# Optimization experiments

Measured on AMD Instinct MI355X. Metric: run time of the kernel, lower is better.

## Reference

```python
import jax, jax.numpy as jnp
import numpy as np

MARGIN = 0.3


def setup_inputs() -> dict:
    key = jax.random.key(0)
    k1, k2 = jax.random.split(key)
    embeddings = jax.random.normal(k1, (128, 512, 1024), dtype=jnp.float32)
    labels = jax.random.randint(k2, (128, 512), 0, 2, dtype=jnp.int64)
    return {"embeddings": embeddings, "labels": labels}


def reference(embeddings, labels):
    # L2-normalize each item embedding (F.normalize, dim=-1)
    emb = embeddings / jnp.linalg.norm(embeddings, axis=-1, keepdims=True)  # [B,N,D]
    dt = emb.dtype

    # Per-sample cosine similarity matrices.
    sim = jnp.einsum('bnd,bmd->bnm', emb, emb)  # [B,N,N]
    diag = jnp.einsum('bnd,bnd->bn', emb, emb)  # [B,N], ~1 after normalization

    pos = labels == 1
    neg = labels == 0
    posf = pos.astype(dt)  # [B,N]
    negf = neg.astype(dt)
    n_pos = pos.sum(-1)  # [B]
    n_neg = neg.sum(-1)

    # Mean similarity of each positive anchor to the OTHER positives
    # (exclude self via diag; original concatenates around p_idx).
    pos_sum = jnp.einsum('bnm,bm->bn', sim, posf) - diag  # [B,N]
    denom_pos = jnp.maximum(n_pos[:, None].astype(dt) - 1, 1)
    pos_sim = jnp.where(n_pos[:, None] > 1, pos_sum / denom_pos, jnp.asarray(1.0, dt))  # [B,N]

    # relu(neg_sim - pos_sim + margin), mean over negatives per anchor.
    tri = jax.nn.relu(sim - pos_sim[:, :, None] + MARGIN)  # [B,N,N]
    denom_neg = jnp.maximum(n_neg[:, None].astype(dt), 1)
    neg_mean = jnp.einsum('bnm,bm->bn', tri, negf) / denom_neg  # [B,N]

    # Only samples with both positives and negatives contribute; one term per positive anchor.
    valid = (n_pos > 0) & (n_neg > 0)  # [B]
    anchor_w = posf * valid[:, None].astype(dt)  # [B,N]
    total = (neg_mean * anchor_w).sum()
    count = (n_pos * valid).sum()
    return total / jnp.maximum(count, 1).astype(dt)
```

## Files before the change

kernel.cpp:

```cpp
#include <hip/hip_runtime.h>
#include <hip/hip_bf16.h>

#define BB 128
#define NN 512
#define DD 1024
#define MARGIN 0.3f

typedef __attribute__((ext_vector_type(8))) short bf16x8;
typedef __attribute__((ext_vector_type(4))) float f32x4;
typedef __attribute__((ext_vector_type(8))) unsigned short ushort8;
typedef long i64f8;

__device__ __forceinline__ unsigned short f2bf(float f) {
    unsigned int u = __float_as_uint(f);
    u += 0x7FFFu + ((u >> 16) & 1u);
    return (unsigned short)(u >> 16);
}
__device__ __forceinline__ int read_label(const unsigned int* lab, int is64, int idx) {
    return (int)(is64 ? lab[2 * idx] : lab[idx]);
}
__device__ __forceinline__ void gload_lds16(const void* g, void* l) {
    __builtin_amdgcn_global_load_lds(
        (const __attribute__((address_space(1))) unsigned int*)g,
        (__attribute__((address_space(3))) unsigned int*)l, 16, 0, 0);
}


__global__ __launch_bounds__(512) void k_compact2(const unsigned int* __restrict__ lab,
                                                  int* __restrict__ slotOf,
                                                  int* __restrict__ counts) {
    int b = blockIdx.x, t = threadIdx.x;
    int lnk = t & 63, wv = t >> 6;

    unsigned int odd = (t < 256) ? lab[2 * (b * 256 + t) + 1] : 0u;
    #pragma unroll
    for (int off = 32; off; off >>= 1) odd |= __shfl_xor(odd, off);
    __shared__ unsigned int ow[8];
    if (lnk == 0) ow[wv] = odd;
    __syncthreads();
    unsigned int tot = ow[0] | ow[1] | ow[2] | ow[3] | ow[4] | ow[5] | ow[6] | ow[7];
    int is64 = (tot == 0) ? 1 : 0;

    int lv = read_label(lab, is64, b * NN + t);
    unsigned long long bp = __ballot(lv == 1);
    int prefP = __popcll(bp & ((1ull << lnk) - 1ull));
    __shared__ int wcP[8];
    if (lnk == 0) wcP[wv] = __popcll(bp);
    __syncthreads();
    int baseP = 0, totP = 0;
    #pragma unroll
    for (int w = 0; w < 8; ++w) {
        int c = wcP[w];
        if (w < wv) baseP += c;
        totP += c;
    }
    int baseN = wv * 64 - baseP;
    int prefN = lnk - prefP;
    int slot = (lv == 1) ? (baseP + prefP) : (totP + baseN + prefN);
    slotOf[b * NN + t] = slot;
    if (t == 0) { counts[2 * b] = totP; counts[2 * b + 1] = NN - totP; }
}

#define TM 128
#define TN 128
__global__ __launch_bounds__(128) void k_tiles(const int* __restrict__ counts,
                                               int* __restrict__ tileList,
                                               int* __restrict__ nTiles) {
    int b = threadIdx.x;
    int P = counts[2 * b], Q = counts[2 * b + 1];
    int nm = (P > 0) ? (P + TM - 1) / TM : 0;
    int nn = (Q > 0) ? (Q + TN - 1) / TN : 0;
    int cnt = nm * nn;
    __shared__ int pre[128];
    pre[b] = cnt;
    __syncthreads();
    for (int d = 1; d < 128; d <<= 1) {
        int v = (b >= d) ? pre[b - d] : 0;
        __syncthreads();
        pre[b] += v;
        __syncthreads();
    }
    int off = pre[b] - cnt;
    for (int mt = 0; mt < nm; ++mt)
        for (int nt = 0; nt < nn; ++nt)
            tileList[off++] = (b << 8) | (mt << 4) | nt;
    if (b == 127) nTiles[0] = pre[127];
}

__global__ __launch_bounds__(256) void k_normcvt(const float* __restrict__ x,
                                                 const int* __restrict__ slotOf,
                                                 unsigned char* __restrict__ y8) {
    int wid = blockIdx.x * 4 + (threadIdx.x >> 6);
    int ln = threadIdx.x & 63;
    const f32x4* src = (const f32x4*)(x + (size_t)wid * DD);
    f32x4 v[4];
    float ss = 0.f;
    #pragma unroll
    for (int j = 0; j < 4; ++j) {
        v[j] = __builtin_nontemporal_load(&src[ln + 64 * j]);
        ss += v[j].x * v[j].x + v[j].y * v[j].y + v[j].z * v[j].z + v[j].w * v[j].w;
    }
    #pragma unroll
    for (int off = 32; off; off >>= 1) ss += __shfl_xor(ss, off);
    float r = rsqrtf(ss);
    int b = wid >> 9;
    int slot = slotOf[wid];
    unsigned char* dst = y8 + ((size_t)(b * NN) + slot) * DD;
    #pragma unroll
    for (int j = 0; j < 4; ++j) {
        int w = 0;
        w = __builtin_amdgcn_cvt_pk_fp8_f32(v[j].x * r, v[j].y * r, w, false);
        w = __builtin_amdgcn_cvt_pk_fp8_f32(v[j].z * r, v[j].w * r, w, true);
        *(unsigned int*)&dst[4 * (ln + 64 * j)] = (unsigned int)w;
    }
}

__global__ __launch_bounds__(256) void k_spos2(const unsigned char* __restrict__ y8,
                                               const int* __restrict__ counts,
                                               float* __restrict__ sposPart) {
    int blk = blockIdx.x;
    int b = blk >> 3, sub = blk & 7;
    int t = threadIdx.x, wv = t >> 6, ln = t & 63;
    int P = counts[2 * b];
    int lo = (sub * P) >> 3, hi = ((sub + 1) * P) >> 3;
    const unsigned char* yb = y8 + (size_t)b * NN * DD;
    float acc[16];
    #pragma unroll
    for (int e = 0; e < 16; ++e) acc[e] = 0.f;
    for (int s = lo + wv; s < hi; s += 4) {
        uint4 w = *(const uint4*)(yb + (size_t)s * DD + 16 * ln);
        unsigned int wa[4] = {w.x, w.y, w.z, w.w};
        #pragma unroll
        for (int i = 0; i < 4; ++i) {
            acc[4 * i + 0] += __builtin_amdgcn_cvt_f32_fp8(wa[i], 0);
            acc[4 * i + 1] += __builtin_amdgcn_cvt_f32_fp8(wa[i], 1);
            acc[4 * i + 2] += __builtin_amdgcn_cvt_f32_fp8(wa[i], 2);
            acc[4 * i + 3] += __builtin_amdgcn_cvt_f32_fp8(wa[i], 3);
        }
    }
    __shared__ float part[4][1024];
    #pragma unroll
    for (int i = 0; i < 4; ++i)
        *(float4*)&part[wv][16 * ln + 4 * i] =
            make_float4(acc[4 * i], acc[4 * i + 1], acc[4 * i + 2], acc[4 * i + 3]);
    __syncthreads();
    float* outp = sposPart + (size_t)blk * DD;
    #pragma unroll
    for (int g = 0; g < 4; ++g) {
        int c = t + 256 * g;
        outp[c] = part[0][c] + part[1][c] + part[2][c] + part[3][c];
    }
}

#define BKG 64

__global__ __launch_bounds__(256) void k_gemm2(const unsigned char* __restrict__ y8,
                                               const float* __restrict__ sposPart,
                                               const int* __restrict__ counts,
                                               const int* __restrict__ tileList,
                                               const int* __restrict__ nTiles,
                                               float* __restrict__ partials) {
    int ticket = blockIdx.x;
    if (ticket >= nTiles[0]) return;
    int tid = threadIdx.x;
    int wv = tid >> 6, ln = tid & 63;

    __shared__ unsigned char As[3 * TM * BKG];
    __shared__ unsigned char Bs[3 * TN * BKG];
    __shared__ unsigned int spos8[DD / 4];
    __shared__ float psA[TM];
    __shared__ float red[4];

    int desc = tileList[ticket];
    int b = desc >> 8, mt = (desc >> 4) & 15, nt = desc & 15;
    int P = counts[2 * b], Q = counts[2 * b + 1];

    {
        const float* base = sposPart + (size_t)(b * 8) * DD + 4 * tid;
        float4 s = {0.f, 0.f, 0.f, 0.f};
        #pragma unroll
        for (int p = 0; p < 8; ++p) {
            float4 v = *(const float4*)(base + (size_t)p * DD);
            s.x += v.x; s.y += v.y; s.z += v.z; s.w += v.w;
        }
        int w = 0;
        w = __builtin_amdgcn_cvt_pk_fp8_f32(s.x, s.y, w, false);
        w = __builtin_amdgcn_cvt_pk_fp8_f32(s.z, s.w, w, true);
        spos8[tid] = (unsigned int)w;
    }
    asm volatile("s_waitcnt lgkmcnt(0)" ::: "memory");
    __builtin_amdgcn_sched_barrier(0);

    const unsigned char* yb = y8 + (size_t)b * NN * DD;
    int arow0 = mt * TM;
    int brow0 = P + nt * TN;

    int rr = ln >> 2;
    int sw9s = (rr & 3) ^ ((rr >> 2) & 3);
    int cbS = ((ln & 3) ^ sw9s) * 16;
    int rA[2], rB[2];
    #pragma unroll
    for (int g = 0; g < 2; ++g) {
        int ran = arow0 + wv * 32 + g * 16 + rr;
        rA[g] = (ran > NN - 1) ? (NN - 1) : ran;
        int rbn = brow0 + wv * 32 + g * 16 + rr;
        rB[g] = (rbn > NN - 1) ? (NN - 1) : rbn;
    }

#define STAGE(bufsel, kk)                                                      \
    {                                                                          \
        _Pragma("unroll")                                                      \
        for (int g_ = 0; g_ < 2; ++g_) {                                       \
            gload_lds16(yb + (size_t)rA[g_] * DD + (kk) + cbS,                 \
                        &As[(bufsel) * TM * BKG + (wv * 32 + g_ * 16) * BKG]); \
            gload_lds16(yb + (size_t)rB[g_] * DD + (kk) + cbS,                 \
                        &Bs[(bufsel) * TN * BKG + (wv * 32 + g_ * 16) * BKG]); \
        }                                                                      \
    }

    int wr = (wv >> 1) * 64, wc = (wv & 1) * 64;
    int fr = ln & 15;
    int swf = (fr & 3) ^ ((fr >> 2) & 3);
    int c0 = ln >> 4;
    bool col0 = (fr == 0);

    f32x4 acc[4][4];
    #pragma unroll
    for (int m = 0; m < 4; ++m)
        #pragma unroll
        for (int n = 0; n < 4; ++n)
            acc[m][n] = (f32x4){0.f, 0.f, 0.f, 0.f};
    f32x4 accE[4];
    #pragma unroll
    for (int m = 0; m < 4; ++m) accE[m] = (f32x4){0.f, 0.f, 0.f, 0.f};

#define COMPUTE(cur, kbase)                                                    \
    {                                                                          \
        i64f8 af[2][4], bfv[2][4], sx[2];                                      \
        _Pragma("unroll")                                                      \
        for (int ks = 0; ks < 2; ++ks) {                                       \
            int cc = c0 + 4 * ks;                                              \
            int off = (((cc >> 1) ^ swf) * 16) + ((cc & 1) * 8);               \
            _Pragma("unroll")                                                  \
            for (int m = 0; m < 4; ++m)                                        \
                af[ks][m] = *(const i64f8*)&As[(cur) * TM * BKG +              \
                                               (wr + m * 16 + fr) * BKG + off];\
            _Pragma("unroll")                                                  \
            for (int n = 0; n < 4; ++n)                                        \
                bfv[ks][n] = *(const i64f8*)&Bs[(cur) * TN * BKG +             \
                                                (wc + n * 16 + fr) * BKG + off];\
            i64f8 sv = *(const i64f8*)&((const unsigned char*)spos8)[(kbase) + \
                                                                     cc * 8];  \
            sx[ks] = col0 ? sv : (i64f8)0;                                     \
        }                                                                      \
        __builtin_amdgcn_s_setprio(1);                                         \
        _Pragma("unroll")                                                      \
        for (int ks = 0; ks < 2; ++ks) {                                       \
            _Pragma("unroll")                                                  \
            for (int m = 0; m < 4; ++m)                                        \
                _Pragma("unroll")                                              \
                for (int n = 0; n < 4; ++n)                                    \
                    acc[m][n] = __builtin_amdgcn_mfma_f32_16x16x32_fp8_fp8(    \
                        af[ks][m], bfv[ks][n], acc[m][n], 0, 0, 0);            \
            _Pragma("unroll")                                                  \
            for (int m = 0; m < 4; ++m)                                        \
                accE[m] = __builtin_amdgcn_mfma_f32_16x16x32_fp8_fp8(          \
                    af[ks][m], sx[ks], accE[m], 0, 0, 0);                      \
        }                                                                      \
        __builtin_amdgcn_s_setprio(0);                                         \
    }

    STAGE(0, 0);
    STAGE(1, BKG);
    STAGE(2, 2 * BKG);

    int cur = 0;
    for (int t = 0; t < 16; ++t) {
        if (t < 14)       asm volatile("s_waitcnt vmcnt(8)" ::: "memory");
        else if (t == 14) asm volatile("s_waitcnt vmcnt(4)" ::: "memory");
        else              asm volatile("s_waitcnt vmcnt(0)" ::: "memory");
        __builtin_amdgcn_s_barrier();
        __builtin_amdgcn_sched_barrier(0);
        COMPUTE(cur, t * BKG);
        __builtin_amdgcn_s_barrier();
        __builtin_amdgcn_sched_barrier(0);
        if (t < 13) STAGE(cur, (t + 3) * BKG);
        cur = (cur == 2) ? 0 : cur + 1;
    }
#undef STAGE
#undef COMPUTE

    float invPm1 = (P > 1) ? 1.0f / (float)(P - 1) : 0.f;
    if (col0 && (wv & 1) == 0) {
        int r0 = (ln >> 4) * 4;
        #pragma unroll
        for (int m = 0; m < 4; ++m)
            #pragma unroll
            for (int q = 0; q < 4; ++q)
                psA[wr + m * 16 + r0 + q] =
                    (P > 1) ? (accE[m][q] - 1.0f) * invPm1 : 1.0f;
    }
    __syncthreads();

    float lsum = 0.f;
    int irow0 = wr + (ln >> 4) * 4;
    #pragma unroll
    for (int m = 0; m < 4; ++m) {
        #pragma unroll
        for (int n = 0; n < 4; ++n) {
            int j = wc + fr + n * 16;
            bool jok = (nt * TN + j) < Q;
            #pragma unroll
            for (int q = 0; q < 4; ++q) {
                int i = irow0 + m * 16 + q;
                float v = fmaxf(acc[m][n][q] - psA[i] + MARGIN, 0.f);
                bool iok = (mt * TM + i) < P;
                lsum += (iok && jok) ? v : 0.f;
            }
        }
    }
    #pragma unroll
    for (int off = 32; off; off >>= 1) lsum += __shfl_xor(lsum, off);
    if (ln == 0) red[wv] = lsum;
    __syncthreads();
    if (tid == 0) partials[ticket] = (red[0] + red[1] + red[2] + red[3]) / (float)Q;
}

__global__ __launch_bounds__(256) void k_final(const float* __restrict__ partials,
                                               const int* __restrict__ nTiles,
                                               const int* __restrict__ counts,
                                               float* __restrict__ out) {
    int t = threadIdx.x;
    int A = nTiles[0];
    float s = 0.f;
    for (int i = t; i < A; i += 256) s += partials[i];
    int c = 0;
    for (int b = t; b < BB; b += 256) {
        int P = counts[2 * b], Q = counts[2 * b + 1];
        if (P > 0 && Q > 0) c += P;
    }
    #pragma unroll
    for (int off = 32; off; off >>= 1) {
        s += __shfl_xor(s, off);
        c += __shfl_xor(c, off);
    }
    __shared__ float rs[4];
    __shared__ int ri[4];
    if ((t & 63) == 0) { rs[t >> 6] = s; ri[t >> 6] = c; }
    __syncthreads();
    if (t == 0) {
        float st = rs[0] + rs[1] + rs[2] + rs[3];
        int ct = ri[0] + ri[1] + ri[2] + ri[3];
        out[0] = st / (float)(ct < 1 ? 1 : ct);
    }
}


__global__ __launch_bounds__(256) void k_detect(const unsigned int* __restrict__ lab,
                                                int* __restrict__ flag) {
    int t = threadIdx.x;
    unsigned int acc = 0;
    for (int i = t; i < 32768; i += 256) acc |= lab[2 * i + 1];
    #pragma unroll
    for (int off = 32; off; off >>= 1) acc |= __shfl_xor(acc, off);
    __shared__ unsigned int w[4];
    if ((t & 63) == 0) w[t >> 6] = acc;
    __syncthreads();
    if (t == 0) flag[0] = ((w[0] | w[1] | w[2] | w[3]) == 0) ? 1 : 0;
}

__global__ __launch_bounds__(256) void k_norm_spos(const float* __restrict__ x,
                                                   const unsigned int* __restrict__ lab,
                                                   const int* __restrict__ flag,
                                                   float* __restrict__ rnorm,
                                                   float* __restrict__ sposPart) {
    int blk = blockIdx.x;
    int b = blk >> 2, sub = blk & 3;
    int t = threadIdx.x;
    int m0 = sub * 128;
    __shared__ float rn[128];
    __shared__ int lb[128];
    const float* xb = x + (size_t)b * NN * DD;
    int is64 = flag[0];
    int wv = t >> 6, ln = t & 63;
    for (int r = wv; r < 128; r += 4) {
        const float4* row = (const float4*)(xb + (size_t)(m0 + r) * DD);
        float s = 0.f;
        #pragma unroll
        for (int k = 0; k < 4; ++k) {
            float4 v = row[ln + 64 * k];
            s += v.x * v.x + v.y * v.y + v.z * v.z + v.w * v.w;
        }
        #pragma unroll
        for (int off = 32; off; off >>= 1) s += __shfl_xor(s, off);
        if (ln == 0) {
            float r_ = rsqrtf(s);
            rn[r] = r_;
            rnorm[b * NN + m0 + r] = r_;
        }
    }
    if (t < 128) lb[t] = read_label(lab, is64, b * NN + m0 + t);
    __syncthreads();
    float s0 = 0.f, s1 = 0.f, s2 = 0.f, s3 = 0.f;
    for (int m = 0; m < 128; ++m) {
        if (lb[m] == 1) {
            float rr = rn[m];
            const float* xr = xb + (size_t)(m0 + m) * DD;
            s0 += xr[t] * rr; s1 += xr[t + 256] * rr;
            s2 += xr[t + 512] * rr; s3 += xr[t + 768] * rr;
        }
    }
    float* sp = sposPart + (size_t)blk * DD;
    sp[t] = s0; sp[t + 256] = s1; sp[t + 512] = s2; sp[t + 768] = s3;
}

__global__ __launch_bounds__(512) void k_compact_fb(const unsigned int* __restrict__ lab,
                                                    const int* __restrict__ flag,
                                                    int* __restrict__ posIdx,
                                                    int* __restrict__ negIdx,
                                                    int* __restrict__ counts) {
    int b = blockIdx.x;
    int t = threadIdx.x;
    __shared__ int pidx[NN], nidx[NN];
    __shared__ int cP, cN;
    if (t == 0) { cP = 0; cN = 0; }
    __syncthreads();
    int lv = read_label(lab, flag[0], b * NN + t);
    if (lv == 1)      { int p = atomicAdd(&cP, 1); pidx[p] = t; }
    else if (lv == 0) { int q = atomicAdd(&cN, 1); nidx[q] = t; }
    __syncthreads();
    posIdx[b * NN + t] = (t < cP) ? pidx[t] : 0;
    negIdx[b * NN + t] = (t < cN) ? nidx[t] : 0;
    if (t == 0) { counts[2 * b] = cP; counts[2 * b + 1] = cN; }
}

__global__ __launch_bounds__(256) void k_possim_fb(const float* __restrict__ x,
                                                   const float* __restrict__ rnorm,
                                                   const float* __restrict__ sposPart,
                                                   const int* __restrict__ posIdx,
                                                   const int* __restrict__ counts,
                                                   float* __restrict__ posSimC) {
    int wid = (blockIdx.x * blockDim.x + threadIdx.x) >> 6;
    int ln = threadIdx.x & 63;
    int b = wid >> 9, i = wid & 511;
    int P = counts[2 * b];
    if (i >= P) { if (ln == 0) posSimC[b * NN + i] = 0.f; return; }
    int n = posIdx[b * NN + i];
    const float* xr = x + ((size_t)b * NN + n) * DD;
    const float* sp = sposPart + (size_t)(b * 4) * DD;
    float s = 0.f;
    #pragma unroll
    for (int k = 0; k < 16; ++k) {
        int c = ln + 64 * k;
        float spv = sp[c] + sp[c + DD] + sp[c + 2 * DD] + sp[c + 3 * DD];
        s += xr[c] * spv;
    }
    #pragma unroll
    for (int off = 32; off; off >>= 1) s += __shfl_xor(s, off);
    if (ln == 0) {
        float ps = (P > 1) ? (s * rnorm[b * NN + n] - 1.0f) / (float)(P - 1) : 1.0f;
        posSimC[b * NN + i] = ps;
    }
}

#define LDST 40
#define FTM 128
#define FTN 128
__global__ __launch_bounds__(256) void k_gemm_fb(const float* __restrict__ x,
                                                 const float* __restrict__ rnorm,
                                                 const int* __restrict__ posIdx,
                                                 const int* __restrict__ negIdx,
                                                 const float* __restrict__ posSimC,
                                                 const int* __restrict__ counts,
                                                 float* __restrict__ partials) {
    int blk = blockIdx.x;
    int b = blk >> 4;
    int mt = (blk >> 2) & 3, nt = blk & 3;
    int tid = threadIdx.x;
    int P = counts[2 * b], Q = counts[2 * b + 1];
    if (mt * FTM >= P || nt * FTN >= Q) {
        if (tid == 0) partials[blk] = 0.f;
        return;
    }
    __shared__ unsigned short As[FTM * LDST];
    __shared__ unsigned short Bs[FTN * LDST];
    __shared__ float rnA[FTM], rnB[FTN], psA[FTM];
    __shared__ int gA[FTM], gB[FTN];
    __shared__ float red[4];
    if (tid < FTM) {
        int gi = posIdx[b * NN + mt * FTM + tid];
        gA[tid] = gi;
        rnA[tid] = rnorm[b * NN + gi];
        psA[tid] = posSimC[b * NN + mt * FTM + tid];
    } else {
        int j = tid - FTM;
        int gj = negIdx[b * NN + nt * FTN + j];
        gB[j] = gj;
        rnB[j] = rnorm[b * NN + gj];
    }
    __syncthreads();
    int sr = tid >> 1, sh = tid & 1;
    const float* xb = x + (size_t)b * NN * DD;
    const float* pa = xb + (size_t)gA[sr] * DD + sh * 16;
    const float* pb = xb + (size_t)gB[sr] * DD + sh * 16;
    unsigned short* wa = &As[sr * LDST + sh * 16];
    unsigned short* wb = &Bs[sr * LDST + sh * 16];
    int wv = tid >> 6, ln = tid & 63;
    int wr = (wv >> 1) * 64, wc = (wv & 1) * 64;
    int fr = ln & 15;
    int kh = (ln >> 4) * 8;
    f32x4 acc[4][4];
    #pragma unroll
    for (int m = 0; m < 4; ++m)
        #pragma unroll
        for (int n = 0; n < 4; ++n)
            acc[m][n] = (f32x4){0.f, 0.f, 0.f, 0.f};
    float4 la[4], lbv[4];
    #pragma unroll
    for (int j = 0; j < 4; ++j) {
        la[j]  = *(const float4*)(pa + 4 * j);
        lbv[j] = *(const float4*)(pb + 4 * j);
    }
    for (int k0 = 0; k0 < DD; k0 += 32) {
        ushort8 ua0 = {f2bf(la[0].x), f2bf(la[0].y), f2bf(la[0].z), f2bf(la[0].w),
                       f2bf(la[1].x), f2bf(la[1].y), f2bf(la[1].z), f2bf(la[1].w)};
        ushort8 ua1 = {f2bf(la[2].x), f2bf(la[2].y), f2bf(la[2].z), f2bf(la[2].w),
                       f2bf(la[3].x), f2bf(la[3].y), f2bf(la[3].z), f2bf(la[3].w)};
        ushort8 ub0 = {f2bf(lbv[0].x), f2bf(lbv[0].y), f2bf(lbv[0].z), f2bf(lbv[0].w),
                       f2bf(lbv[1].x), f2bf(lbv[1].y), f2bf(lbv[1].z), f2bf(lbv[1].w)};
        ushort8 ub1 = {f2bf(lbv[2].x), f2bf(lbv[2].y), f2bf(lbv[2].z), f2bf(lbv[2].w),
                       f2bf(lbv[3].x), f2bf(lbv[3].y), f2bf(lbv[3].z), f2bf(lbv[3].w)};
        __syncthreads();
        *(ushort8*)wa = ua0; *(ushort8*)(wa + 8) = ua1;
        *(ushort8*)wb = ub0; *(ushort8*)(wb + 8) = ub1;
        __syncthreads();
        if (k0 + 32 < DD) {
            #pragma unroll
            for (int j = 0; j < 4; ++j) {
                la[j]  = *(const float4*)(pa + k0 + 32 + 4 * j);
                lbv[j] = *(const float4*)(pb + k0 + 32 + 4 * j);
            }
        }
        bf16x8 af[4], bfv[4];
        #pragma unroll
        for (int m = 0; m < 4; ++m)
            af[m] = *(const bf16x8*)&As[(wr + m * 16 + fr) * LDST + kh];
        #pragma unroll
        for (int n = 0; n < 4; ++n)
            bfv[n] = *(const bf16x8*)&Bs[(wc + n * 16 + fr) * LDST + kh];
        #pragma unroll
        for (int m = 0; m < 4; ++m)
            #pragma unroll
            for (int n = 0; n < 4; ++n)
                acc[m][n] = __builtin_amdgcn_mfma_f32_16x16x32_bf16(af[m], bfv[n], acc[m][n], 0, 0, 0);
    }
    float lsum = 0.f;
    int irow0 = wr + (ln >> 4) * 4;
    #pragma unroll
    for (int m = 0; m < 4; ++m) {
        #pragma unroll
        for (int n = 0; n < 4; ++n) {
            int j = wc + fr + n * 16;
            float rbn = rnB[j];
            bool jok = (nt * FTN + j) < Q;
            #pragma unroll
            for (int q = 0; q < 4; ++q) {
                int i = irow0 + m * 16 + q;
                float v = fmaxf(acc[m][n][q] * rnA[i] * rbn - psA[i] + MARGIN, 0.f);
                bool iok = (mt * FTM + i) < P;
                lsum += (iok && jok) ? v : 0.f;
            }
        }
    }
    #pragma unroll
    for (int off = 32; off; off >>= 1) lsum += __shfl_xor(lsum, off);
    if (ln == 0) red[wv] = lsum;
    __syncthreads();
    if (tid == 0) partials[blk] = (red[0] + red[1] + red[2] + red[3]) / (float)Q;
}

__global__ __launch_bounds__(256) void k_final_fb(const float* __restrict__ partials,
                                                  const int* __restrict__ counts,
                                                  float* __restrict__ out) {
    int t = threadIdx.x;
    float s = 0.f;
    for (int i = t; i < BB * 16; i += 256) s += partials[i];
    int c = 0;
    for (int b = t; b < BB; b += 256) {
        int P = counts[2 * b], Q = counts[2 * b + 1];
        if (P > 0 && Q > 0) c += P;
    }
    #pragma unroll
    for (int off = 32; off; off >>= 1) {
        s += __shfl_xor(s, off);
        c += __shfl_xor(c, off);
    }
    __shared__ float rs[4];
    __shared__ int ri[4];
    if ((t & 63) == 0) { rs[t >> 6] = s; ri[t >> 6] = c; }
    __syncthreads();
    if (t == 0) {
        float st = rs[0] + rs[1] + rs[2] + rs[3];
        int ct = ri[0] + ri[1] + ri[2] + ri[3];
        out[0] = st / (float)(ct < 1 ? 1 : ct);
    }
}

extern "C" void kernel_launch(void* const* d_in, const int* in_sizes, int n_in,
                              void* d_out, int out_size, void* d_ws, size_t ws_size,
                              hipStream_t stream) {
    const float* x = (const float*)d_in[0];
    const unsigned int* lab = (const unsigned int*)d_in[1];
    char* ws = (char*)d_ws;
    float* out = (float*)d_out;

    const size_t Y_BYTES = (size_t)BB * NN * DD;
    const size_t O_SLOT  = Y_BYTES;
    const size_t O_CNT   = O_SLOT + 262144;
    const size_t O_SPOS  = O_CNT + 1024;
    const size_t O_PART  = O_SPOS + 4194304;
    const size_t O_TILE  = O_PART + 16384;
    const size_t O_NT    = O_TILE + 8192;
    const size_t NEED    = O_NT + 64;

    if (ws_size >= NEED) {
        unsigned char* y8 = (unsigned char*)ws;
        int*   slotOf   = (int*)(ws + O_SLOT);
        int*   counts   = (int*)(ws + O_CNT);
        float* sposPart = (float*)(ws + O_SPOS);
        float* partials = (float*)(ws + O_PART);
        int*   tileList = (int*)(ws + O_TILE);
        int*   nTiles   = (int*)(ws + O_NT);

        k_compact2<<<BB, 512, 0, stream>>>(lab, slotOf, counts);
        k_tiles<<<1, 128, 0, stream>>>(counts, tileList, nTiles);
        k_normcvt<<<16384, 256, 0, stream>>>(x, slotOf, y8);
        k_spos2<<<BB * 8, 256, 0, stream>>>(y8, counts, sposPart);
        k_gemm2<<<2048, 256, 0, stream>>>(y8, sposPart, counts, tileList, nTiles, partials);
        k_final<<<1, 256, 0, stream>>>(partials, nTiles, counts, out);
    } else {
        float* rnorm    = (float*)(ws + 0);
        int*   posIdx   = (int*)(ws + 262144);
        int*   negIdx   = (int*)(ws + 524288);
        float* posSimC  = (float*)(ws + 786432);
        float* sposPart = (float*)(ws + 1048576);
        int*   counts   = (int*)(ws + 3145728);
        float* partials = (float*)(ws + 3146752);
        int*   flag     = (int*)(ws + 3154944);

        k_detect<<<1, 256, 0, stream>>>(lab, flag);
        k_norm_spos<<<BB * 4, 256, 0, stream>>>(x, lab, flag, rnorm, sposPart);
        k_compact_fb<<<BB, 512, 0, stream>>>(lab, flag, posIdx, negIdx, counts);
        k_possim_fb<<<16384, 256, 0, stream>>>(x, rnorm, sposPart, posIdx, counts, posSimC);
        k_gemm_fb<<<BB * 16, 256, 0, stream>>>(x, rnorm, posIdx, negIdx, posSimC, counts, partials);
        k_final_fb<<<1, 256, 0, stream>>>(partials, counts, out);
    }
}
```

Before: 118.5 us.

## Pre-swizzle fp8 rows in global memory and pad negatives to fixed offset

The normalize/convert kernel now writes each fp8 row with an 8-byte-chunk XOR swizzle keyed on the row index, so the GEMM tile loader can copy contiguous 16-byte chunks straight into LDS and the fragment reads still avoid bank conflicts. This replaces the swizzle that was previously computed at load time. The per-sample buffer is doubled to 1024 rows so negatives always start at row 512, which makes B-tile row addressing independent of the positive count. The cost is twice the workspace for the fp8 copy and extra index arithmetic in the positive-sum kernel.

```diff
diff --git a/kernel.cpp b/kernel.cpp
--- a/kernel.cpp
+++ b/kernel.cpp
@@ -3,6 +3,7 @@
 
 #define BB 128
 #define NN 512
+#define NR 1024
 #define DD 1024
 #define MARGIN 0.3f
 
@@ -56,7 +57,7 @@
     }
     int baseN = wv * 64 - baseP;
     int prefN = lnk - prefP;
-    int slot = (lv == 1) ? (baseP + prefP) : (totP + baseN + prefN);
+    int slot = (lv == 1) ? (baseP + prefP) : (512 + baseN + prefN);
     slotOf[b * NN + t] = slot;
     if (t == 0) { counts[2 * b] = totP; counts[2 * b + 1] = NN - totP; }
 }
@@ -104,14 +105,18 @@
     for (int off = 32; off; off >>= 1) ss += __shfl_xor(ss, off);
     float r = rsqrtf(ss);
     int b = wid >> 9;
-    int slot = slotOf[wid];
-    unsigned char* dst = y8 + ((size_t)(b * NN) + slot) * DD;
+    int phys = slotOf[wid];
+    unsigned char* dst = y8 + ((size_t)b * NR + phys) * DD;
+    int w = (phys >> 1) & 7;
     #pragma unroll
     for (int j = 0; j < 4; ++j) {
-        int w = 0;
-        w = __builtin_amdgcn_cvt_pk_fp8_f32(v[j].x * r, v[j].y * r, w, false);
-        w = __builtin_amdgcn_cvt_pk_fp8_f32(v[j].z * r, v[j].w * r, w, true);
-        *(unsigned int*)&dst[4 * (ln + 64 * j)] = (unsigned int)w;
+        int wd = 0;
+        wd = __builtin_amdgcn_cvt_pk_fp8_f32(v[j].x * r, v[j].y * r, wd, false);
+        wd = __builtin_amdgcn_cvt_pk_fp8_f32(v[j].z * r, v[j].w * r, wd, true);
+        int p = ln + 64 * j;
+        int c = p >> 1;
+        int cp = (c & ~7) | ((c & 7) ^ w);
+        *(unsigned int*)&dst[cp * 8 + (p & 1) * 4] = (unsigned int)wd;
     }
 }
 
@@ -123,13 +128,18 @@
     int t = threadIdx.x, wv = t >> 6, ln = t & 63;
     int P = counts[2 * b];
     int lo = (sub * P) >> 3, hi = ((sub + 1) * P) >> 3;
-    const unsigned char* yb = y8 + (size_t)b * NN * DD;
+    const unsigned char* yb = y8 + (size_t)b * NR * DD;
+    int u = 2 * (ln & 3);
+    int blockoff = (ln >> 2) * 64;
     float acc[16];
     #pragma unroll
     for (int e = 0; e < 16; ++e) acc[e] = 0.f;
     for (int s = lo + wv; s < hi; s += 4) {
-        uint4 w = *(const uint4*)(yb + (size_t)s * DD + 16 * ln);
-        unsigned int wa[4] = {w.x, w.y, w.z, w.w};
+        int w = (s >> 1) & 7;
+        const unsigned char* rowp = yb + (size_t)s * DD + blockoff;
+        uint2 a8 = *(const uint2*)(rowp + ((u ^ w) * 8));
+        uint2 b8 = *(const uint2*)(rowp + (((u + 1) ^ w) * 8));
+        unsigned int wa[4] = {a8.x, a8.y, b8.x, b8.y};
         #pragma unroll
         for (int i = 0; i < 4; ++i) {
             acc[4 * i + 0] += __builtin_amdgcn_cvt_f32_fp8(wa[i], 0);
@@ -191,20 +201,18 @@
     asm volatile("s_waitcnt lgkmcnt(0)" ::: "memory");
     __builtin_amdgcn_sched_barrier(0);
 
-    const unsigned char* yb = y8 + (size_t)b * NN * DD;
+    const unsigned char* yb = y8 + (size_t)b * NR * DD;
     int arow0 = mt * TM;
-    int brow0 = P + nt * TN;
-
+    int brow0 = 512 + nt * TN;
     int rr = ln >> 2;
-    int sw9s = (rr & 3) ^ ((rr >> 2) & 3);
-    int cbS = ((ln & 3) ^ sw9s) * 16;
+    int cbS = (ln & 3) * 16;
     int rA[2], rB[2];
     #pragma unroll
     for (int g = 0; g < 2; ++g) {
         int ran = arow0 + wv * 32 + g * 16 + rr;
-        rA[g] = (ran > NN - 1) ? (NN - 1) : ran;
+        rA[g] = (ran > 511) ? 511 : ran;
         int rbn = brow0 + wv * 32 + g * 16 + rr;
-        rB[g] = (rbn > NN - 1) ? (NN - 1) : rbn;
+        rB[g] = (rbn > NR - 1) ? (NR - 1) : rbn;
     }
 
 #define STAGE(bufsel, kk)                                                      \
@@ -220,7 +228,7 @@
 
     int wr = (wv >> 1) * 64, wc = (wv & 1) * 64;
     int fr = ln & 15;
-    int swf = (fr & 3) ^ ((fr >> 2) & 3);
+    int wfr = (fr >> 1) & 7;
     int c0 = ln >> 4;
     bool col0 = (fr == 0);
 
@@ -240,7 +248,7 @@
         _Pragma("unroll")                                                      \
         for (int ks = 0; ks < 2; ++ks) {                                       \
             int cc = c0 + 4 * ks;                                              \
-            int off = (((cc >> 1) ^ swf) * 16) + ((cc & 1) * 8);               \
+            int off = (cc ^ wfr) * 8;                                          \
             _Pragma("unroll")                                                  \
             for (int m = 0; m < 4; ++m)                                        \
                 af[ks][m] = *(const i64f8*)&As[(cur) * TM * BKG +              \
@@ -614,7 +622,7 @@
     char* ws = (char*)d_ws;
     float* out = (float*)d_out;
 
-    const size_t Y_BYTES = (size_t)BB * NN * DD;
+    const size_t Y_BYTES = (size_t)BB * NR * DD;
     const size_t O_SLOT  = Y_BYTES;
     const size_t O_CNT   = O_SLOT + 262144;
     const size_t O_SPOS  = O_CNT + 1024;
```

Measured after the change: 120.1 us. About the same (+1.3%).
